# Optimization experiments

Hardware: AMD Instinct MI355X
Metric: run time of the kernel (lower is better)

## Reference

```python
import jax, jax.numpy as jnp
from jax import lax
import numpy as np

IMG = 2048.0            # square image size (W=H)
STRIDES = [32, 64, 128]
FEATS = [64, 32, 16]    # IMG / stride
NUM_CLASSES = 80
BATCH = 8
SCORE_THRESH = 0.2
NMS_THRESH = 0.6
TOPK = 1000             # topk_candidates per level
DETS = 100              # detections_per_img


def make_anchors(fs, stride):
    # square anchors of size==stride centered on the feature grid (AnchorGenerator with ratio 1.0)
    c = (jnp.arange(fs, dtype=jnp.float32) + 0.5) * stride
    cy, cx = jnp.meshgrid(c, c, indexing='ij')
    cx, cy = cx.reshape(-1), cy.reshape(-1)
    h = stride / 2.0
    return jnp.stack([cx - h, cy - h, cx + h, cy + h], axis=1)


def setup_inputs() -> dict:
    key = jax.random.key(0)
    inp = {}
    for i, (fs, s) in enumerate(zip(FEATS, STRIDES)):
        hw = fs * fs
        key, k1, k2, k3 = jax.random.split(key, 4)
        inp[f'cls{i}'] = jax.random.normal(k1, (BATCH, hw, NUM_CLASSES), jnp.float32)
        inp[f'reg{i}'] = jax.random.uniform(k2, (BATCH, hw, 4), jnp.float32)
        inp[f'ctr{i}'] = jax.random.normal(k3, (BATCH, hw), jnp.float32)
        inp[f'anc{i}'] = make_anchors(fs, float(s))
    return inp


def _decode(rel, boxes):
    # BoxLinearCoder.decode_single with normalize_by_size=True
    cx = 0.5 * (boxes[:, 0] + boxes[:, 2])
    cy = 0.5 * (boxes[:, 1] + boxes[:, 3])
    w = boxes[:, 2] - boxes[:, 0]
    h = boxes[:, 3] - boxes[:, 1]
    rel = rel * jnp.stack([w, h, w, h], axis=1)
    return jnp.stack([cx - rel[:, 0], cy - rel[:, 1], cx + rel[:, 2], cy + rel[:, 3]], axis=1)


def _iou(b):
    # torchvision box_iou on a single set of boxes [N,4] -> [N,N]
    area = (b[:, 2] - b[:, 0]) * (b[:, 3] - b[:, 1])
    lt = jnp.maximum(b[:, None, :2], b[None, :, :2])
    rb = jnp.minimum(b[:, None, 2:], b[None, :, 2:])
    wh = jnp.clip(rb - lt, 0.0)
    inter = wh[..., 0] * wh[..., 1]
    return inter / (area[:, None] + area[None, :] - inter)


def _greedy_keep(iou):
    # classic greedy NMS on score-sorted boxes: suppress j>i with iou>thresh if i kept
    n = iou.shape[0]
    idx = jnp.arange(n)
    def body(i, keep):
        supp = keep[i] & (iou[i] > NMS_THRESH) & (idx > i)
        return keep & ~supp
    return lax.fori_loop(0, n, body, jnp.ones((n,), bool))


def _per_image(cls_l, reg_l, ctr_l, anc_l):
    boxes, scores, labels = [], [], []
    for cls, reg, ctr, anc in zip(cls_l, reg_l, ctr_l, anc_l):
        hw, c = cls.shape
        # scores = sqrt(sigmoid(cls) * sigmoid(ctrness)) flattened over anchors*classes
        sc = jnp.sqrt(jax.nn.sigmoid(cls) * jax.nn.sigmoid(ctr)[:, None]).reshape(-1)
        sc = jnp.where(sc > SCORE_THRESH, sc, -1.0)  # score threshold as mask (static shapes)
        ts, ti = lax.top_k(sc, TOPK)                 # per-level top-k candidates
        aidx = ti // c
        lab = ti % c
        b = jnp.clip(_decode(reg[aidx], anc[aidx]), 0.0, IMG)  # decode + clip to image
        boxes.append(b); scores.append(ts); labels.append(lab)
    boxes = jnp.concatenate(boxes)    # [3*TOPK, 4]
    scores = jnp.concatenate(scores)  # [3*TOPK]
    labels = jnp.concatenate(labels)  # [3*TOPK]
    n = scores.shape[0]
    # batched_nms via per-class coordinate offsets
    off = labels.astype(boxes.dtype) * (IMG + 1.0)
    ss, oi = lax.top_k(scores, n)     # sort candidates by score desc
    bs = boxes[oi] + off[oi][:, None]
    keep = lax.stop_gradient(_greedy_keep(_iou(bs)))
    fsc = jnp.where(keep & (ss > 0), ss, -1.0)
    fs, fi = lax.top_k(fsc, DETS)     # keep detections_per_img; score==-1 marks padding
    return boxes[oi][fi], fs, labels[oi][fi]


def reference(cls0, cls1, cls2, reg0, reg1, reg2, ctr0, ctr1, ctr2, anc0, anc1, anc2):
    f = jax.vmap(lambda c0, c1, c2, r0, r1, r2, t0, t1, t2: _per_image(
        [c0, c1, c2], [r0, r1, r2], [t0, t1, t2], [anc0, anc1, anc2]))
    return f(cls0, cls1, cls2, reg0, reg1, reg2, ctr0, ctr1, ctr2)
```

## Files before the change

kernel.cpp:

```cpp
#include <hip/hip_runtime.h>

#define NCLS  80
#define TOPK  1000
#define NLVL  3
#define NIMG  8
#define NCAND 3000
#define DETS  100
#define CAP   2048
#define HBINS 4096
#define NHBLK 16
#define NCBLK 64
#define GATH  512
#define QBASE 0x3F800000u
#define QMAX  0x41C80000u
#define IMGSZ 2048.0f


__device__ __forceinline__ float sigm(float x) {
    if (x >= 0.f) return 1.f / (1.f + expf(-x));
    float e = expf(x);
    return e / (1.f + e);
}

__device__ __forceinline__ unsigned int qbits(float ea, float t1) {
    return __float_as_uint(__fmul_rn(__fadd_rn(1.f, ea), t1));
}

__device__ __forceinline__ void bitonic_desc(unsigned long long* s, int N) {
    for (int k = 2; k <= N; k <<= 1) {
        for (int j = k >> 1; j > 0; j >>= 1) {
            __syncthreads();
            for (int i = threadIdx.x; i < N; i += blockDim.x) {
                int ixj = i ^ j;
                if (ixj > i) {
                    unsigned long long a = s[i], b = s[ixj];
                    bool up = ((i & k) == 0);
                    if (up ? (a < b) : (a > b)) { s[i] = b; s[ixj] = a; }
                }
            }
        }
    }
    __syncthreads();
}

__device__ __forceinline__ void lvl_select(int level,
    const float* c0, const float* c1, const float* c2,
    const float* t0, const float* t1, const float* t2,
    const float** cls, const float** ctr, int* hw) {
    if (level == 0)      { *cls = c0; *ctr = t0; *hw = 4096; }
    else if (level == 1) { *cls = c1; *ctr = t1; *hw = 1024; }
    else                 { *cls = c2; *ctr = t2; *hw = 256; }
}


__global__ void k_hist(const float* c0, const float* c1, const float* c2,
                       const float* t0, const float* t1, const float* t2,
                       unsigned int* parts) {
    int level = blockIdx.z, img = blockIdx.y;
    const float* cls; const float* ctr; int hw;
    lvl_select(level, c0, c1, c2, t0, t1, t2, &cls, &ctr, &hw);
    int n4 = hw * (NCLS / 4);
    const float4* cl4 = (const float4*)(cls + (size_t)img * hw * NCLS);
    const float* ct = ctr + (size_t)img * hw;
    __shared__ unsigned int h[HBINS];
    for (int i = threadIdx.x; i < HBINS; i += 256) h[i] = 0;
    __syncthreads();
    for (int i = blockIdx.x * 256 + threadIdx.x; i < n4; i += NHBLK * 256) {
        float4 v = cl4[i];
        int a = i / (NCLS / 4);
        float eb = expf(-ct[a]);
        float t1 = __fadd_rn(1.f, eb);
        #pragma unroll
        for (int k = 0; k < 4; ++k) {
            float x = (k == 0) ? v.x : (k == 1) ? v.y : (k == 2) ? v.z : v.w;
            unsigned int qb = qbits(expf(-x), t1);
            if (qb < QMAX) {
                unsigned int bin = (qb - QBASE) >> 13;
                if (bin > HBINS - 1) bin = HBINS - 1;
                atomicAdd(&h[bin], 1u);
            }
        }
    }
    __syncthreads();
    unsigned int* P = parts + ((size_t)((img * NLVL + level) * NHBLK + blockIdx.x)) * HBINS;
    for (int i = threadIdx.x; i < HBINS; i += 256) P[i] = h[i];
}


__global__ void k_find(const unsigned int* parts, unsigned int* vcut) {
    int pair = blockIdx.x;
    int tid = threadIdx.x;
    __shared__ unsigned int hb[HBINS];
    __shared__ unsigned int segsum[256];
    __shared__ unsigned int pref[256];
    unsigned int acc[HBINS / 256];
    #pragma unroll
    for (int j = 0; j < HBINS / 256; ++j) acc[j] = 0;
    for (int blk = 0; blk < NHBLK; ++blk) {
        const unsigned int* P = parts + ((size_t)(pair * NHBLK + blk)) * HBINS;
        #pragma unroll
        for (int j = 0; j < HBINS / 256; ++j) acc[j] += P[tid + 256 * j];
    }
    #pragma unroll
    for (int j = 0; j < HBINS / 256; ++j) hb[tid + 256 * j] = acc[j];
    __syncthreads();
    unsigned int seg = 0;
    #pragma unroll
    for (int j = 0; j < 16; ++j) seg += hb[16 * tid + j];
    segsum[tid] = seg;
    pref[tid] = seg;
    __syncthreads();
    for (int off = 1; off < 256; off <<= 1) {
        unsigned int v = (tid >= off) ? pref[tid - off] : 0u;
        __syncthreads();
        pref[tid] += v;
        __syncthreads();
    }
    unsigned int incl = pref[tid];
    unsigned int excl = incl - seg;
    if (excl < (unsigned int)TOPK && incl >= (unsigned int)TOPK) {
        unsigned int cum = excl; int B = HBINS - 1;
        for (int b = 16 * tid; b < 16 * tid + 16; ++b) {
            cum += hb[b];
            if (cum >= (unsigned int)TOPK) { B = b; break; }
        }
        vcut[pair] = (B >= HBINS - 1) ? QMAX : (QBASE + ((unsigned int)(B + 1) << 13));
    }
    if (tid == 255 && pref[255] < (unsigned int)TOPK)
        vcut[pair] = QMAX;
}


__global__ void k_collect(const float* c0, const float* c1, const float* c2,
                          const float* t0, const float* t1, const float* t2,
                          const unsigned int* vcut, unsigned int* counters,
                          unsigned long long* buf) {
    int level = blockIdx.z, img = blockIdx.y;
    const float* cls; const float* ctr; int hw;
    lvl_select(level, c0, c1, c2, t0, t1, t2, &cls, &ctr, &hw);
    int n4 = hw * (NCLS / 4);
    int pair = img * NLVL + level;
    const float4* cl4 = (const float4*)(cls + (size_t)img * hw * NCLS);
    const float* ct = ctr + (size_t)img * hw;
    unsigned int V = vcut[pair];
    __shared__ unsigned long long sbuf[2048];
    __shared__ unsigned int scnt;
    __shared__ unsigned int sbase;
    if (threadIdx.x == 0) scnt = 0;
    __syncthreads();
    for (int i = blockIdx.x * 256 + threadIdx.x; i < n4; i += NCBLK * 256) {
        float4 v = cl4[i];
        int a = i / (NCLS / 4);
        float cta = ct[a];
        float eb = expf(-cta);
        float t1 = __fadd_rn(1.f, eb);
        #pragma unroll
        for (int k = 0; k < 4; ++k) {
            float x = (k == 0) ? v.x : (k == 1) ? v.y : (k == 2) ? v.z : v.w;
            unsigned int qb = qbits(expf(-x), t1);
            if (qb < V) {
                float s = sqrtf(sigm(x) * sigm(cta));
                unsigned int e = (unsigned int)(4 * i + k);
                unsigned int slot = atomicAdd(&scnt, 1u);
                if (slot < 2048)
                    sbuf[slot] = ((unsigned long long)__float_as_uint(s) << 32) | (~e);
            }
        }
    }
    __syncthreads();
    unsigned int cl_n = scnt; if (cl_n > 2048) cl_n = 2048;
    if (threadIdx.x == 0)
        sbase = atomicAdd(&counters[pair * 16], cl_n);
    __syncthreads();
    unsigned int base = sbase;
    for (unsigned int idx = threadIdx.x; idx < cl_n; idx += 256) {
        unsigned int g = base + idx;
        if (g < CAP) buf[(size_t)pair * CAP + g] = sbuf[idx];
    }
}


__global__ void __launch_bounds__(1024)
k_sort_pairs(const unsigned long long* buf, const unsigned int* counters,
             const float* r0, const float* r1, const float* r2,
             const float* a0, const float* a1, const float* a2,
             float* cand_box, int* cand_lab, unsigned long long* gkey) {
    int pair = blockIdx.x;
    int img = pair / NLVL, level = pair % NLVL;
    __shared__ unsigned long long s[CAP];
    int cnt = (int)counters[pair * 16]; if (cnt > CAP) cnt = CAP;
    for (int i = threadIdx.x; i < CAP; i += blockDim.x)
        s[i] = (i < cnt) ? buf[(size_t)pair * CAP + i] : 0ull;
    bitonic_desc(s, CAP);
    const float* reg; const float* anc; int hw;
    if (level == 0)      { reg = r0; anc = a0; hw = 4096; }
    else if (level == 1) { reg = r1; anc = a1; hw = 1024; }
    else                 { reg = r2; anc = a2; hw = 256; }
    const float* rg = reg + (size_t)img * hw * 4;
    for (int r = threadIdx.x; r < TOPK; r += blockDim.x) {
        unsigned long long key = s[r];
        int cpos = level * TOPK + r;
        size_t o = (size_t)img * NCAND + cpos;
        float b0 = 0, b1 = 0, b2 = 0, b3 = 0; int lab = 0; unsigned int bits = 0;
        if (key != 0ull) {
            bits = (unsigned int)(key >> 32);
            unsigned int idx = ~((unsigned int)key);
            int a = (int)(idx / NCLS); lab = (int)(idx % NCLS);
            float ax1 = anc[a * 4 + 0], ay1 = anc[a * 4 + 1];
            float ax2 = anc[a * 4 + 2], ay2 = anc[a * 4 + 3];
            float cx = 0.5f * (ax1 + ax2), cy = 0.5f * (ay1 + ay2);
            float w = ax2 - ax1, h = ay2 - ay1;
            float e0 = rg[a * 4 + 0] * w, e1 = rg[a * 4 + 1] * h;
            float e2 = rg[a * 4 + 2] * w, e3 = rg[a * 4 + 3] * h;
            b0 = fminf(fmaxf(cx - e0, 0.f), IMGSZ);
            b1 = fminf(fmaxf(cy - e1, 0.f), IMGSZ);
            b2 = fminf(fmaxf(cx + e2, 0.f), IMGSZ);
            b3 = fminf(fmaxf(cy + e3, 0.f), IMGSZ);
        }
        cand_box[o * 4 + 0] = b0; cand_box[o * 4 + 1] = b1;
        cand_box[o * 4 + 2] = b2; cand_box[o * 4 + 3] = b3;
        cand_lab[o] = lab;
        gkey[o] = ((unsigned long long)bits << 32) | (unsigned int)(~((unsigned int)cpos));
    }
}


__global__ void __launch_bounds__(1024)
k_merge_nms(const unsigned long long* gkey, const float* cand_box, const int* cand_lab,
            float* out) {
    int img = blockIdx.x;
    int tid = threadIdx.x;
    __shared__ unsigned long long A[TOPK], B[TOPK], C[TOPK];
    __shared__ unsigned long long M[2 * TOPK];
    __shared__ unsigned long long S[NCAND];
    __shared__ float4 wbox[GATH];
    __shared__ int    wlab[GATH];
    __shared__ float4 sbx[64]; __shared__ float sar[64];
    __shared__ float4 koff[DETS]; __shared__ float karr[DETS];
    __shared__ float4 kb[DETS]; __shared__ float ks[DETS]; __shared__ int kl[DETS];
    __shared__ float4 rb[DETS]; __shared__ int rl[DETS];

    const unsigned long long* G = gkey + (size_t)img * NCAND;
    for (int i = tid; i < TOPK; i += 1024) { A[i] = G[i]; B[i] = G[TOPK + i]; C[i] = G[2 * TOPK + i]; }
    __syncthreads();

    for (int k = tid; k < 2 * TOPK; k += 1024) {
        int lo = max(0, k - TOPK), hi = min(k, TOPK);
        while (lo < hi) {
            int mid = (lo + hi) >> 1;
            if (A[mid] > B[k - mid - 1]) lo = mid + 1; else hi = mid;
        }
        int i = lo, j = k - lo;
        unsigned long long av = (i < TOPK) ? A[i] : 0ull;
        unsigned long long bv = (j < TOPK) ? B[j] : 0ull;
        M[k] = (av > bv) ? av : bv;
    }
    __syncthreads();
    for (int k = tid; k < NCAND; k += 1024) {
        int lo = max(0, k - TOPK), hi = min(k, 2 * TOPK);
        while (lo < hi) {
            int mid = (lo + hi) >> 1;
            if (M[mid] > C[k - mid - 1]) lo = mid + 1; else hi = mid;
        }
        int i = lo, j = k - lo;
        unsigned long long mv = (i < 2 * TOPK) ? M[i] : 0ull;
        unsigned long long cv = (j < TOPK) ? C[j] : 0ull;
        S[k] = (mv > cv) ? mv : cv;
    }
    __syncthreads();

    const float4* CB4 = (const float4*)cand_box + (size_t)img * NCAND;
    const int* CL = cand_lab + (size_t)img * NCAND;
    if (tid < GATH) {
        unsigned int pos = ~((unsigned int)S[tid]);
        float4 b4 = make_float4(0.f, 0.f, 0.f, 0.f); int lbv = 0;
        if (pos < NCAND) { b4 = CB4[pos]; lbv = CL[pos]; }
        wbox[tid] = b4; wlab[tid] = lbv;
    }
    __syncthreads();

    if (tid >= 64) return;
    int lane = tid;
    unsigned long long lmask_lt = (lane == 0) ? 0ull : (~0ull >> (64 - lane));

    int kept = 0, ring = 0, r = 0;

    while (kept < DETS && r < NCAND) {
        int rank = r + lane;
        unsigned long long key = (rank < NCAND) ? S[rank] : 0ull;
        unsigned int bits = (unsigned int)(key >> 32);
        unsigned long long pm = __ballot(bits != 0u);
        int npos = (pm == ~0ull) ? 64 : (int)__builtin_ctzll(~pm);
        if (npos == 0) break;

        float4 bx = make_float4(0.f, 0.f, 0.f, 0.f); int lb = 0;
        if (lane < npos) {
            unsigned int pos = ~((unsigned int)key);
            if (rank < GATH) { bx = wbox[rank]; lb = wlab[rank]; }
            else if (pos < NCAND) { bx = CB4[pos]; lb = CL[pos]; }
        }
        float off = (float)lb * (IMGSZ + 1.0f);
        float ox1 = bx.x + off, oy1 = bx.y + off;
        float ox2 = bx.z + off, oy2 = bx.w + off;
        float car = (ox2 - ox1) * (oy2 - oy1);
        sbx[lane] = make_float4(ox1, oy1, ox2, oy2);
        sar[lane] = car;

        bool supk = false;
        for (int k2 = 0; k2 < kept; ++k2) {
            float4 kk = koff[k2]; float ka = karr[k2];
            float lx = fmaxf(kk.x, ox1), ly = fmaxf(kk.y, oy1);
            float rx = fminf(kk.z, ox2), ry = fminf(kk.w, oy2);
            float w = fmaxf(rx - lx, 0.f), h = fmaxf(ry - ly, 0.f);
            float inter = w * h;
            supk = supk || (inter / (ka + car - inter) > 0.6f);
        }
        unsigned long long col = 0ull;
        for (int i = 0; i < npos; ++i) {
            float4 c = sbx[i]; float ca = sar[i];
            float lx = fmaxf(c.x, ox1), ly = fmaxf(c.y, oy1);
            float rx = fminf(c.z, ox2), ry = fminf(c.w, oy2);
            float w = fmaxf(rx - lx, 0.f), h = fmaxf(ry - ly, 0.f);
            float inter = w * h;
            if ((inter / (ca + car - inter) > 0.6f) && (i < lane)) col |= (1ull << i);
        }
        unsigned long long undecided = __ballot((lane < npos) && !supk);
        unsigned long long aliveSel = 0ull;
        int capleft = DETS - kept;
        int lastSlot = npos - 1;
        while (undecided) {
            int i = (int)__builtin_ctzll(undecided);
            aliveSel |= (1ull << i);
            undecided &= ~(1ull << i);
            if (--capleft == 0) { lastSlot = i; break; }
            unsigned long long row = __ballot(((col >> i) & 1ull) != 0ull);
            undecided &= ~row;
        }
        unsigned long long region = (lastSlot >= 63) ? ~0ull : ((1ull << (lastSlot + 1)) - 1ull);
        region &= (npos >= 64) ? ~0ull : ((1ull << npos) - 1ull);
        unsigned long long rejm = region & ~aliveSel;

        if ((aliveSel >> lane) & 1ull) {
            int ki = kept + (int)__popcll(aliveSel & lmask_lt);
            koff[ki] = make_float4(ox1, oy1, ox2, oy2); karr[ki] = car;
            kb[ki] = bx; ks[ki] = __uint_as_float(bits); kl[ki] = lb;
        }
        if ((rejm >> lane) & 1ull) {
            int ri = ring + (int)__popcll(rejm & lmask_lt);
            if (ri < DETS) { rb[ri] = bx; rl[ri] = lb; }
        }
        kept += (int)__popcll(aliveSel);
        ring += (int)__popcll(rejm);
        r += lastSlot + 1;
    }

    while (kept < DETS && ring < DETS && r < NCAND) {
        int rank = r + lane;
        if (rank < NCAND) {
            int ri = ring + lane;
            if (ri < DETS) {
                unsigned long long key = S[rank];
                unsigned int pos = ~((unsigned int)key);
                float4 bx = make_float4(0.f, 0.f, 0.f, 0.f); int lb = 0;
                if (rank < GATH) { bx = wbox[rank]; lb = wlab[rank]; }
                else if (pos < NCAND) { bx = CB4[pos]; lb = CL[pos]; }
                rb[ri] = bx; rl[ri] = lb;
            }
        }
        int take = NCAND - r; if (take > 64) take = 64;
        ring += take;
        r += 64;
    }

    for (int k = lane; k < DETS; k += 64) {
        float4 bxo; float scv; int lv;
        if (k < kept) { bxo = kb[k]; scv = ks[k]; lv = kl[k]; }
        else { int q = k - kept; bxo = rb[q]; scv = -1.0f; lv = rl[q]; }
        float* ob = out + ((size_t)img * DETS + k) * 4;
        ob[0] = bxo.x; ob[1] = bxo.y; ob[2] = bxo.z; ob[3] = bxo.w;
        out[NIMG * DETS * 4 + img * DETS + k] = scv;
        out[NIMG * DETS * 5 + img * DETS + k] = (float)lv;
    }
}


extern "C" void kernel_launch(void* const* d_in, const int* in_sizes, int n_in,
                              void* d_out, int out_size, void* d_ws, size_t ws_size,
                              hipStream_t stream) {
    (void)in_sizes; (void)n_in; (void)out_size; (void)ws_size;
    const float* cls0 = (const float*)d_in[0];
    const float* reg0 = (const float*)d_in[1];
    const float* ctr0 = (const float*)d_in[2];
    const float* anc0 = (const float*)d_in[3];
    const float* cls1 = (const float*)d_in[4];
    const float* reg1 = (const float*)d_in[5];
    const float* ctr1 = (const float*)d_in[6];
    const float* anc1 = (const float*)d_in[7];
    const float* cls2 = (const float*)d_in[8];
    const float* reg2 = (const float*)d_in[9];
    const float* ctr2 = (const float*)d_in[10];
    const float* anc2 = (const float*)d_in[11];
    float* out = (float*)d_out;
    char* ws = (char*)d_ws;

    const size_t OFF_PARTS = 0;
    const size_t OFF_CNT   = 6291456;
    const size_t ZERO_OFF  = 6291456;
    const size_t ZERO_B    = 1536;
    const size_t OFF_VCUT  = 6292992;
    const size_t OFF_BUF   = 6293120;
    const size_t OFF_CBOX  = 6686336;
    const size_t OFF_CLAB  = 7070336;
    const size_t OFF_GKEY  = 7166336;

    unsigned int* parts = (unsigned int*)(ws + OFF_PARTS);
    unsigned int* cnt   = (unsigned int*)(ws + OFF_CNT);
    unsigned int* vcut  = (unsigned int*)(ws + OFF_VCUT);
    unsigned long long* buf  = (unsigned long long*)(ws + OFF_BUF);
    float* cand_box = (float*)(ws + OFF_CBOX);
    int*   cand_lab = (int*)(ws + OFF_CLAB);
    unsigned long long* gkey = (unsigned long long*)(ws + OFF_GKEY);

    hipMemsetAsync(ws + ZERO_OFF, 0, ZERO_B, stream);

    k_hist<<<dim3(NHBLK, NIMG, NLVL), 256, 0, stream>>>(cls0, cls1, cls2, ctr0, ctr1, ctr2, parts);
    k_find<<<24, 256, 0, stream>>>(parts, vcut);
    k_collect<<<dim3(NCBLK, NIMG, NLVL), 256, 0, stream>>>(cls0, cls1, cls2, ctr0, ctr1, ctr2,
                                                           vcut, cnt, buf);
    k_sort_pairs<<<24, 1024, 0, stream>>>(buf, cnt, reg0, reg1, reg2, anc0, anc1, anc2,
                                          cand_box, cand_lab, gkey);
    k_merge_nms<<<NIMG, 1024, 0, stream>>>(gkey, cand_box, cand_lab, out);
}
```

Before: 178.9 us.

## Fuse histogram+find and collect+sort kernels using last-block-done counters

Merges k_hist with k_find and k_collect with k_sort_pairs. Each block bumps a per-pair atomic done counter, and the last block to finish does the reduction or the bitonic sort, so two kernel launches and their gaps go away. The collect kernel now runs 16 blocks of 1024 threads per pair instead of 64 of 256. In exchange, the final step runs serially inside one block after the others finish, and correctness relies on threadfence ordering plus extra zeroed counters in the workspace.

```diff
diff --git a/kernel.cpp b/kernel.cpp
--- a/kernel.cpp
+++ b/kernel.cpp
@@ -9,7 +9,7 @@
 #define CAP   2048
 #define HBINS 4096
 #define NHBLK 16
-#define NCBLK 64
+#define NCBLK 16
 #define GATH  512
 #define QBASE 0x3F800000u
 #define QMAX  0x41C80000u
@@ -53,16 +53,20 @@
 }
 
 
-__global__ void k_hist(const float* c0, const float* c1, const float* c2,
-                       const float* t0, const float* t1, const float* t2,
-                       unsigned int* parts) {
+__global__ void k_hist_find(const float* c0, const float* c1, const float* c2,
+                            const float* t0, const float* t1, const float* t2,
+                            unsigned int* parts, unsigned int* done1, unsigned int* vcut) {
     int level = blockIdx.z, img = blockIdx.y;
+    int pair = img * NLVL + level;
     const float* cls; const float* ctr; int hw;
     lvl_select(level, c0, c1, c2, t0, t1, t2, &cls, &ctr, &hw);
     int n4 = hw * (NCLS / 4);
     const float4* cl4 = (const float4*)(cls + (size_t)img * hw * NCLS);
     const float* ct = ctr + (size_t)img * hw;
     __shared__ unsigned int h[HBINS];
+    __shared__ unsigned int flag;
+    __shared__ unsigned int segsum[256];
+    __shared__ unsigned int pref[256];
     for (int i = threadIdx.x; i < HBINS; i += 256) h[i] = 0;
     __syncthreads();
     for (int i = blockIdx.x * 256 + threadIdx.x; i < n4; i += NHBLK * 256) {
@@ -82,31 +86,28 @@
         }
     }
     __syncthreads();
-    unsigned int* P = parts + ((size_t)((img * NLVL + level) * NHBLK + blockIdx.x)) * HBINS;
+    unsigned int* P = parts + ((size_t)(pair * NHBLK + blockIdx.x)) * HBINS;
     for (int i = threadIdx.x; i < HBINS; i += 256) P[i] = h[i];
-}
-
-
-__global__ void k_find(const unsigned int* parts, unsigned int* vcut) {
-    int pair = blockIdx.x;
+    __threadfence();
+    if (threadIdx.x == 0) flag = atomicAdd(&done1[pair * 16], 1u);
+    __syncthreads();
+    if (flag != NHBLK - 1) return;
+    __threadfence();
     int tid = threadIdx.x;
-    __shared__ unsigned int hb[HBINS];
-    __shared__ unsigned int segsum[256];
-    __shared__ unsigned int pref[256];
     unsigned int acc[HBINS / 256];
     #pragma unroll
     for (int j = 0; j < HBINS / 256; ++j) acc[j] = 0;
     for (int blk = 0; blk < NHBLK; ++blk) {
-        const unsigned int* P = parts + ((size_t)(pair * NHBLK + blk)) * HBINS;
+        const unsigned int* Pb = parts + ((size_t)(pair * NHBLK + blk)) * HBINS;
         #pragma unroll
-        for (int j = 0; j < HBINS / 256; ++j) acc[j] += P[tid + 256 * j];
+        for (int j = 0; j < HBINS / 256; ++j) acc[j] += Pb[tid + 256 * j];
     }
     #pragma unroll
-    for (int j = 0; j < HBINS / 256; ++j) hb[tid + 256 * j] = acc[j];
+    for (int j = 0; j < HBINS / 256; ++j) h[tid + 256 * j] = acc[j];
     __syncthreads();
     unsigned int seg = 0;
     #pragma unroll
-    for (int j = 0; j < 16; ++j) seg += hb[16 * tid + j];
+    for (int j = 0; j < 16; ++j) seg += h[16 * tid + j];
     segsum[tid] = seg;
     pref[tid] = seg;
     __syncthreads();
@@ -121,7 +122,7 @@
     if (excl < (unsigned int)TOPK && incl >= (unsigned int)TOPK) {
         unsigned int cum = excl; int B = HBINS - 1;
         for (int b = 16 * tid; b < 16 * tid + 16; ++b) {
-            cum += hb[b];
+            cum += h[b];
             if (cum >= (unsigned int)TOPK) { B = b; break; }
         }
         vcut[pair] = (B >= HBINS - 1) ? QMAX : (QBASE + ((unsigned int)(B + 1) << 13));
@@ -131,24 +132,29 @@
 }
 
 
-__global__ void k_collect(const float* c0, const float* c1, const float* c2,
-                          const float* t0, const float* t1, const float* t2,
-                          const unsigned int* vcut, unsigned int* counters,
-                          unsigned long long* buf) {
+__global__ void __launch_bounds__(1024)
+k_collect_sort(const float* c0, const float* c1, const float* c2,
+               const float* t0, const float* t1, const float* t2,
+               const unsigned int* vcut, unsigned int* counters, unsigned long long* buf,
+               unsigned int* done2,
+               const float* r0, const float* r1, const float* r2,
+               const float* a0, const float* a1, const float* a2,
+               float* cand_box, int* cand_lab, unsigned long long* gkey) {
     int level = blockIdx.z, img = blockIdx.y;
+    int pair = img * NLVL + level;
     const float* cls; const float* ctr; int hw;
     lvl_select(level, c0, c1, c2, t0, t1, t2, &cls, &ctr, &hw);
     int n4 = hw * (NCLS / 4);
-    int pair = img * NLVL + level;
     const float4* cl4 = (const float4*)(cls + (size_t)img * hw * NCLS);
     const float* ct = ctr + (size_t)img * hw;
     unsigned int V = vcut[pair];
-    __shared__ unsigned long long sbuf[2048];
+    __shared__ unsigned long long s[CAP];
     __shared__ unsigned int scnt;
     __shared__ unsigned int sbase;
+    __shared__ unsigned int flag;
     if (threadIdx.x == 0) scnt = 0;
     __syncthreads();
-    for (int i = blockIdx.x * 256 + threadIdx.x; i < n4; i += NCBLK * 256) {
+    for (int i = blockIdx.x * 1024 + threadIdx.x; i < n4; i += NCBLK * 1024) {
         float4 v = cl4[i];
         int a = i / (NCLS / 4);
         float cta = ct[a];
@@ -159,45 +165,39 @@
             float x = (k == 0) ? v.x : (k == 1) ? v.y : (k == 2) ? v.z : v.w;
             unsigned int qb = qbits(expf(-x), t1);
             if (qb < V) {
-                float s = sqrtf(sigm(x) * sigm(cta));
+                float sv = sqrtf(sigm(x) * sigm(cta));
                 unsigned int e = (unsigned int)(4 * i + k);
                 unsigned int slot = atomicAdd(&scnt, 1u);
-                if (slot < 2048)
-                    sbuf[slot] = ((unsigned long long)__float_as_uint(s) << 32) | (~e);
+                if (slot < CAP)
+                    s[slot] = ((unsigned long long)__float_as_uint(sv) << 32) | (~e);
             }
         }
     }
     __syncthreads();
-    unsigned int cl_n = scnt; if (cl_n > 2048) cl_n = 2048;
+    unsigned int cl_n = scnt; if (cl_n > CAP) cl_n = CAP;
     if (threadIdx.x == 0)
         sbase = atomicAdd(&counters[pair * 16], cl_n);
     __syncthreads();
     unsigned int base = sbase;
-    for (unsigned int idx = threadIdx.x; idx < cl_n; idx += 256) {
+    for (unsigned int idx = threadIdx.x; idx < cl_n; idx += 1024) {
         unsigned int g = base + idx;
-        if (g < CAP) buf[(size_t)pair * CAP + g] = sbuf[idx];
-    }
-}
-
-
-__global__ void __launch_bounds__(1024)
-k_sort_pairs(const unsigned long long* buf, const unsigned int* counters,
-             const float* r0, const float* r1, const float* r2,
-             const float* a0, const float* a1, const float* a2,
-             float* cand_box, int* cand_lab, unsigned long long* gkey) {
-    int pair = blockIdx.x;
-    int img = pair / NLVL, level = pair % NLVL;
-    __shared__ unsigned long long s[CAP];
+        if (g < CAP) buf[(size_t)pair * CAP + g] = s[idx];
+    }
+    __threadfence();
+    if (threadIdx.x == 0) flag = atomicAdd(&done2[pair * 16], 1u);
+    __syncthreads();
+    if (flag != NCBLK - 1) return;
+    __threadfence();
     int cnt = (int)counters[pair * 16]; if (cnt > CAP) cnt = CAP;
-    for (int i = threadIdx.x; i < CAP; i += blockDim.x)
+    for (int i = threadIdx.x; i < CAP; i += 1024)
         s[i] = (i < cnt) ? buf[(size_t)pair * CAP + i] : 0ull;
     bitonic_desc(s, CAP);
-    const float* reg; const float* anc; int hw;
-    if (level == 0)      { reg = r0; anc = a0; hw = 4096; }
-    else if (level == 1) { reg = r1; anc = a1; hw = 1024; }
-    else                 { reg = r2; anc = a2; hw = 256; }
+    const float* reg; const float* anc;
+    if (level == 0)      { reg = r0; anc = a0; }
+    else if (level == 1) { reg = r1; anc = a1; }
+    else                 { reg = r2; anc = a2; }
     const float* rg = reg + (size_t)img * hw * 4;
-    for (int r = threadIdx.x; r < TOPK; r += blockDim.x) {
+    for (int r = threadIdx.x; r < TOPK; r += 1024) {
         unsigned long long key = s[r];
         int cpos = level * TOPK + r;
         size_t o = (size_t)img * NCAND + cpos;
@@ -405,16 +405,20 @@
 
     const size_t OFF_PARTS = 0;
     const size_t OFF_CNT   = 6291456;
+    const size_t OFF_DONE1 = 6292992;
+    const size_t OFF_DONE2 = 6294528;
     const size_t ZERO_OFF  = 6291456;
-    const size_t ZERO_B    = 1536;
-    const size_t OFF_VCUT  = 6292992;
-    const size_t OFF_BUF   = 6293120;
-    const size_t OFF_CBOX  = 6686336;
-    const size_t OFF_CLAB  = 7070336;
-    const size_t OFF_GKEY  = 7166336;
+    const size_t ZERO_B    = 4608;
+    const size_t OFF_VCUT  = 6296064;
+    const size_t OFF_BUF   = 6296192;
+    const size_t OFF_CBOX  = 6689408;
+    const size_t OFF_CLAB  = 7073408;
+    const size_t OFF_GKEY  = 7169408;
 
     unsigned int* parts = (unsigned int*)(ws + OFF_PARTS);
     unsigned int* cnt   = (unsigned int*)(ws + OFF_CNT);
+    unsigned int* done1 = (unsigned int*)(ws + OFF_DONE1);
+    unsigned int* done2 = (unsigned int*)(ws + OFF_DONE2);
     unsigned int* vcut  = (unsigned int*)(ws + OFF_VCUT);
     unsigned long long* buf  = (unsigned long long*)(ws + OFF_BUF);
     float* cand_box = (float*)(ws + OFF_CBOX);
@@ -423,11 +427,10 @@
 
     hipMemsetAsync(ws + ZERO_OFF, 0, ZERO_B, stream);
 
-    k_hist<<<dim3(NHBLK, NIMG, NLVL), 256, 0, stream>>>(cls0, cls1, cls2, ctr0, ctr1, ctr2, parts);
-    k_find<<<24, 256, 0, stream>>>(parts, vcut);
-    k_collect<<<dim3(NCBLK, NIMG, NLVL), 256, 0, stream>>>(cls0, cls1, cls2, ctr0, ctr1, ctr2,
-                                                           vcut, cnt, buf);
-    k_sort_pairs<<<24, 1024, 0, stream>>>(buf, cnt, reg0, reg1, reg2, anc0, anc1, anc2,
-                                          cand_box, cand_lab, gkey);
+    k_hist_find<<<dim3(NHBLK, NIMG, NLVL), 256, 0, stream>>>(
+        cls0, cls1, cls2, ctr0, ctr1, ctr2, parts, done1, vcut);
+    k_collect_sort<<<dim3(NCBLK, NIMG, NLVL), 1024, 0, stream>>>(
+        cls0, cls1, cls2, ctr0, ctr1, ctr2, vcut, cnt, buf, done2,
+        reg0, reg1, reg2, anc0, anc1, anc2, cand_box, cand_lab, gkey);
     k_merge_nms<<<NIMG, 1024, 0, stream>>>(gkey, cand_box, cand_lab, out);
 }
```

New measurement: 350.6 us. 95.9% more time.
